# Optimization experiments

Measured on AMD Instinct MI355X. Metric: run time of the kernel, lower is better.

The kernel has to match this reference:

```python
import jax, jax.numpy as jnp
import numpy as np

K = 7
G = 16
PAD = K // 2
EPS = 1e-5


def setup_inputs() -> dict:
    key = jax.random.key(0)
    ks = jax.random.split(key, 8)
    C = 256
    Cr = C // 4  # ratio=4 bottleneck
    inputs = jax.random.normal(ks[0], (4, C, 56, 56), dtype=jnp.float32)
    W1 = jax.random.normal(ks[1], (Cr, C), dtype=jnp.float32) * 0.05
    b1 = jax.random.normal(ks[2], (Cr,), dtype=jnp.float32) * 0.05
    gamma = jax.random.normal(ks[3], (Cr,), dtype=jnp.float32) * 0.1 + 1.0
    beta = jax.random.normal(ks[4], (Cr,), dtype=jnp.float32) * 0.1
    mean = jax.random.normal(ks[5], (Cr,), dtype=jnp.float32) * 0.1
    var = jax.random.uniform(ks[6], (Cr,), dtype=jnp.float32) * 0.5 + 0.5
    W2 = jax.random.normal(ks[7], (G * K * K, Cr), dtype=jnp.float32) * 0.05
    b2 = jnp.zeros((G * K * K,), dtype=jnp.float32)
    return {"inputs": inputs, "W1": W1, "b1": b1, "gamma": gamma,
            "beta": beta, "mean": mean, "var": var, "W2": W2, "b2": b2}


def reference(inputs, W1, b1, gamma, beta, mean, var, W2, b2):
    B, C, H, W = inputs.shape
    Cg = C // G
    # kernel-generation branch: 1x1 conv -> BN (eval stats) -> relu -> 1x1 conv
    t = jnp.einsum('bchw,oc->bohw', inputs, W1) + b1[None, :, None, None]
    scale = gamma / jnp.sqrt(var + EPS)
    t = t * scale[None, :, None, None] + (beta - mean * scale)[None, :, None, None]
    t = jax.nn.relu(t)
    w = jnp.einsum('bchw,oc->bohw', t, W2) + b2[None, :, None, None]
    w = w.reshape(B, G, K * K, H, W)  # per-pixel kernel
    # involution: accumulate shifted slices instead of materializing unfold
    xp = jnp.pad(inputs, ((0, 0), (0, 0), (PAD, PAD), (PAD, PAD)))
    xg = xp.reshape(B, G, Cg, H + 2 * PAD, W + 2 * PAD)
    out = jnp.zeros((B, G, Cg, H, W), dtype=inputs.dtype)
    k = 0
    for i in range(K):
        for j in range(K):
            out = out + xg[:, :, :, i:i + H, j:j + W] * w[:, :, k][:, :, None, :, :]
            k += 1
    return out.reshape(B, C, H, W)
```

## Files before the change

kernel.cpp:

```cpp
#include <hip/hip_runtime.h>

#define HW    3136
#define HDIM  56
#define CIN   256
#define CR    64
#define NG    16
#define KK    49
#define BEPS  1e-5f

#define RB     2
#define NBAND  28
#define CHALF  28
#define WSTR   60
#define XR     8
#define XC     36
#define XCG    16
#define XTOT   (XR * XCG * XC)

typedef __attribute__((ext_vector_type(8))) short short8;
typedef __attribute__((ext_vector_type(4))) float f32x4;

__device__ __forceinline__ unsigned short f2bf(float f) {
    union { float f; unsigned u; } v; v.f = f;
    unsigned r = (v.u + 0x7FFFu + ((v.u >> 16) & 1u)) >> 16;
    return (unsigned short)r;
}

__global__ __launch_bounds__(256) void k0_prep(
    const float* __restrict__ W1, const float* __restrict__ b1,
    const float* __restrict__ gamma, const float* __restrict__ beta,
    const float* __restrict__ mean, const float* __restrict__ var,
    const float* __restrict__ W2,
    unsigned short* __restrict__ W1b, unsigned short* __restrict__ W2bT,
    float* __restrict__ b1f)
{
    int idx = blockIdx.x * 256 + threadIdx.x;
    if (idx < CR * CIN) {
        int o = idx >> 8;
        float s = gamma[o] * rsqrtf(var[o] + BEPS);
        W1b[idx] = f2bf(W1[idx] * s);
    } else if (idx < CR * CIN + NG * 64 * 64) {
        int j = idx - CR * CIN;
        int c = j & 63, tap = (j >> 6) & 63, g = j >> 12;
        float v = (tap < KK) ? W2[(g * KK + tap) * CR + c] : 0.f;
        W2bT[j] = f2bf(v);
    } else if (idx < CR * CIN + NG * 64 * 64 + CR) {
        int o = idx - CR * CIN - NG * 64 * 64;
        float s = gamma[o] * rsqrtf(var[o] + BEPS);
        b1f[o] = b1[o] * s + beta[o] - mean[o] * s;
    }
}

__global__ __launch_bounds__(128) void k1_gemm(
    const float* __restrict__ x, const unsigned short* __restrict__ W1b,
    const float* __restrict__ b1f, unsigned short* __restrict__ t_bf)
{
    __shared__ float red[64 * 17];

    const int tid = threadIdx.x;
    const int b = blockIdx.y;
    const int lane = tid & 63, l15 = lane & 15, q = lane >> 4;
    const int wid = tid >> 6;
    const int pxb = blockIdx.x * 16;
    const int kb = wid * 128;

    const float* xp = x + (size_t)b * CIN * HW + pxb + l15;

    f32x4 acc[4];
#pragma unroll
    for (int nt = 0; nt < 4; nt++) acc[nt] = (f32x4){0.f, 0.f, 0.f, 0.f};

#pragma unroll
    for (int kc = 0; kc < 4; kc++) {
        short8 af;
#pragma unroll
        for (int j = 0; j < 8; j++) {
            float xv = xp[(size_t)(kb + kc * 32 + q * 8 + j) * HW];
            af[j] = (short)f2bf(xv);
        }
#pragma unroll
        for (int nt = 0; nt < 4; nt++) {
            short8 bf = *(const short8*)&W1b[(size_t)(16 * nt + l15) * CIN + kb + kc * 32 + q * 8];
            acc[nt] = __builtin_amdgcn_mfma_f32_16x16x32_bf16(af, bf, acc[nt], 0, 0, 0);
        }
    }

    if (wid == 1) {
#pragma unroll
        for (int nt = 0; nt < 4; nt++)
#pragma unroll
            for (int r = 0; r < 4; r++)
                red[lane * 17 + nt * 4 + r] = acc[nt][r];
    }
    __syncthreads();
    if (wid == 0) {
#pragma unroll
        for (int nt = 0; nt < 4; nt++) {
            float bias = b1f[16 * nt + l15];
#pragma unroll
            for (int r = 0; r < 4; r++) {
                int px = pxb + 4 * q + r;
                float v = acc[nt][r] + red[lane * 17 + nt * 4 + r] + bias;
                t_bf[((size_t)b * HW + px) * CR + 16 * nt + l15] = f2bf(fmaxf(v, 0.f));
            }
        }
    }
}

__global__ __launch_bounds__(256, 5) void k2_fused(
    const float* __restrict__ x, const unsigned short* __restrict__ t_bf,
    const unsigned short* __restrict__ W2bT, const float* __restrict__ b2,
    float* __restrict__ out)
{
    __shared__ float w_lds[KK * WSTR];
    __shared__ float x_lds[XTOT];

    const int tid = threadIdx.x;
    const int band = blockIdx.x >> 1, chalf = blockIdx.x & 1;
    const int g = blockIdx.y, b = blockIdx.z;
    const int h0 = band * RB, c0 = chalf * CHALF;
    const int lane = tid & 63, l15 = lane & 15, q = lane >> 4;
    const int wid = tid >> 6;

#pragma unroll
    for (int it = 0; it < 18; it++) {
        int i = it * 256 + tid;
        int col = i % XC; int t2 = i / XC; int cg = t2 & 15; int rowx = t2 >> 4;
        int hy = h0 - 3 + rowx, xc = c0 + col - 4;
        float v = 0.f;
        if (hy >= 0 && hy < HDIM && xc >= 0 && xc < HDIM)
            v = x[((size_t)b * CIN + g * 16 + cg) * HW + hy * HDIM + xc];
        x_lds[i] = v;
    }

    {
        short8 bfr[4][2];
#pragma unroll
        for (int nt = 0; nt < 4; nt++)
#pragma unroll
            for (int ks = 0; ks < 2; ks++)
                bfr[nt][ks] = *(const short8*)&W2bT[((size_t)g * 64 + 16 * nt + l15) * 64 + ks * 32 + q * 8];
        float b2v[4];
#pragma unroll
        for (int nt = 0; nt < 4; nt++) {
            int tap = 16 * nt + l15;
            b2v[nt] = (tap < KK) ? b2[g * KK + tap] : 0.f;
        }
        const int row = wid >> 1, seg = wid & 1;
        int px = (h0 + row) * HDIM + c0 + seg * 16 + l15;
        if (px > HW - 1) px = HW - 1;
        const unsigned short* tp = &t_bf[((size_t)b * HW + px) * CR];
        short8 a0 = *(const short8*)&tp[q * 8];
        short8 a1 = *(const short8*)&tp[32 + q * 8];
        const int cl = seg * 16 + 4 * q;
#pragma unroll
        for (int nt = 0; nt < 4; nt++) {
            f32x4 acc = (f32x4){0.f, 0.f, 0.f, 0.f};
            acc = __builtin_amdgcn_mfma_f32_16x16x32_bf16(a0, bfr[nt][0], acc, 0, 0, 0);
            acc = __builtin_amdgcn_mfma_f32_16x16x32_bf16(a1, bfr[nt][1], acc, 0, 0, 0);
            int tap = 16 * nt + l15;
            if (tap < KK && cl < CHALF) {
                *(float4*)&w_lds[tap * WSTR + row * CHALF + cl] =
                    make_float4(acc[0] + b2v[nt], acc[1] + b2v[nt],
                                acc[2] + b2v[nt], acc[3] + b2v[nt]);
            }
        }
    }
    __syncthreads();

    if (tid < 224) {
        const int cg   = tid & 15;
        const int rq   = tid >> 4;
        const int row  = rq & 1;
        const int quad = rq >> 1;
        const int colb = quad * 4, h = h0 + row;

        float acc[4] = {0.f, 0.f, 0.f, 0.f};

#pragma unroll
        for (int di = 0; di < 7; di++) {
            float wv[7][4];
#pragma unroll
            for (int dj = 0; dj < 7; dj++) {
                float4 wq = *(const float4*)&w_lds[(di * 7 + dj) * WSTR + row * CHALF + colb];
                wv[dj][0] = wq.x; wv[dj][1] = wq.y; wv[dj][2] = wq.z; wv[dj][3] = wq.w;
            }
            const float* xr = &x_lds[((row + di) * 16 + cg) * XC + colb];
            float4 A  = *(const float4*)&xr[0];
            float4 Bv = *(const float4*)&xr[4];
            float4 Cv = *(const float4*)&xr[8];
            float win[12] = {A.x, A.y, A.z, A.w, Bv.x, Bv.y, Bv.z, Bv.w,
                             Cv.x, Cv.y, Cv.z, Cv.w};
#pragma unroll
            for (int dj = 0; dj < 7; dj++)
#pragma unroll
                for (int kk = 0; kk < 4; kk++)
                    acc[kk] += win[kk + dj + 1] * wv[dj][kk];
        }
        float* op = &out[((size_t)b * CIN + g * 16 + cg) * HW + h * HDIM + c0 + colb];
        *(float4*)op = make_float4(acc[0], acc[1], acc[2], acc[3]);
    }
}

extern "C" void kernel_launch(void* const* d_in, const int* in_sizes, int n_in,
                              void* d_out, int out_size, void* d_ws, size_t ws_size,
                              hipStream_t stream) {
    const float* x     = (const float*)d_in[0];
    const float* W1    = (const float*)d_in[1];
    const float* b1    = (const float*)d_in[2];
    const float* gamma = (const float*)d_in[3];
    const float* beta  = (const float*)d_in[4];
    const float* mean  = (const float*)d_in[5];
    const float* var   = (const float*)d_in[6];
    const float* W2    = (const float*)d_in[7];
    const float* b2    = (const float*)d_in[8];
    float* out = (float*)d_out;

    unsigned short* t_bf = (unsigned short*)d_ws;
    unsigned short* W1b  = t_bf + (size_t)4 * HW * CR;
    unsigned short* W2bT = W1b + CR * CIN;
    float* b1f           = (float*)(W2bT + NG * 64 * 64);

    int n_k0 = CR * CIN + NG * 64 * 64 + CR;
    k0_prep<<<(n_k0 + 255) / 256, 256, 0, stream>>>(
        W1, b1, gamma, beta, mean, var, W2, W1b, W2bT, b1f);

    dim3 g1(HW / 16, 4);
    k1_gemm<<<g1, 128, 0, stream>>>(x, W1b, b1f, t_bf);

    dim3 g2(NBAND * 2, NG, 4);
    k2_fused<<<g2, 256, 0, stream>>>(x, t_bf, W2bT, b2, out);
}
```

Baseline: 127.9 us.

## Fold weight prep into GEMM kernel and vectorize involution halo loads

After: 111.6 us (median of 2 runs). -12.7%, faster.

```diff
diff --git a/kernel.cpp b/kernel.cpp
--- a/kernel.cpp
+++ b/kernel.cpp
@@ -16,6 +16,9 @@
 #define XC     36
 #define XCG    16
 #define XTOT   (XR * XCG * XC)
+#define NSLOT  1152
+#define K1X    (HW / 16)
+#define K1PREP 32
 
 typedef __attribute__((ext_vector_type(8))) short short8;
 typedef __attribute__((ext_vector_type(4))) float f32x4;
@@ -26,39 +29,31 @@
     return (unsigned short)r;
 }
 
-__global__ __launch_bounds__(256) void k0_prep(
-    const float* __restrict__ W1, const float* __restrict__ b1,
-    const float* __restrict__ gamma, const float* __restrict__ beta,
-    const float* __restrict__ mean, const float* __restrict__ var,
-    const float* __restrict__ W2,
-    unsigned short* __restrict__ W1b, unsigned short* __restrict__ W2bT,
-    float* __restrict__ b1f)
+__global__ __launch_bounds__(128) void k1_gemm(
+    const float* __restrict__ x, const float* __restrict__ W1,
+    const float* __restrict__ b1, const float* __restrict__ gamma,
+    const float* __restrict__ beta, const float* __restrict__ mean,
+    const float* __restrict__ var, const float* __restrict__ W2,
+    unsigned short* __restrict__ t_bf, unsigned short* __restrict__ W2bT)
 {
-    int idx = blockIdx.x * 256 + threadIdx.x;
-    if (idx < CR * CIN) {
-        int o = idx >> 8;
-        float s = gamma[o] * rsqrtf(var[o] + BEPS);
-        W1b[idx] = f2bf(W1[idx] * s);
-    } else if (idx < CR * CIN + NG * 64 * 64) {
-        int j = idx - CR * CIN;
-        int c = j & 63, tap = (j >> 6) & 63, g = j >> 12;
-        float v = (tap < KK) ? W2[(g * KK + tap) * CR + c] : 0.f;
-        W2bT[j] = f2bf(v);
-    } else if (idx < CR * CIN + NG * 64 * 64 + CR) {
-        int o = idx - CR * CIN - NG * 64 * 64;
-        float s = gamma[o] * rsqrtf(var[o] + BEPS);
-        b1f[o] = b1[o] * s + beta[o] - mean[o] * s;
-    }
-}
-
-__global__ __launch_bounds__(128) void k1_gemm(
-    const float* __restrict__ x, const unsigned short* __restrict__ W1b,
-    const float* __restrict__ b1f, unsigned short* __restrict__ t_bf)
-{
-    __shared__ float red[64 * 17];
-
     const int tid = threadIdx.x;
     const int b = blockIdx.y;
+
+    if (blockIdx.x >= K1X) {
+        if (b) return;
+        int i = (blockIdx.x - K1X) * 128 + tid;
+#pragma unroll
+        for (int r = 0; r < 16; r++) {
+            int j = r * 4096 + i;
+            int c = j & 63, tap = (j >> 6) & 63, g = j >> 12;
+            float v = (tap < KK) ? W2[((size_t)g * KK + tap) * CR + c] : 0.f;
+            W2bT[j] = f2bf(v);
+        }
+        return;
+    }
+
+    __shared__ float red[64 * 17];
+
     const int lane = tid & 63, l15 = lane & 15, q = lane >> 4;
     const int wid = tid >> 6;
     const int pxb = blockIdx.x * 16;
@@ -66,6 +61,15 @@
 
     const float* xp = x + (size_t)b * CIN * HW + pxb + l15;
 
+    float sc[4], bias[4];
+#pragma unroll
+    for (int nt = 0; nt < 4; nt++) {
+        int o = 16 * nt + l15;
+        float s = gamma[o] * rsqrtf(var[o] + BEPS);
+        sc[nt] = s;
+        bias[nt] = b1[o] * s + beta[o] - mean[o] * s;
+    }
+
     f32x4 acc[4];
 #pragma unroll
     for (int nt = 0; nt < 4; nt++) acc[nt] = (f32x4){0.f, 0.f, 0.f, 0.f};
@@ -74,13 +78,18 @@
     for (int kc = 0; kc < 4; kc++) {
         short8 af;
 #pragma unroll
-        for (int j = 0; j < 8; j++) {
-            float xv = xp[(size_t)(kb + kc * 32 + q * 8 + j) * HW];
-            af[j] = (short)f2bf(xv);
-        }
+        for (int j = 0; j < 8; j++)
+            af[j] = (short)f2bf(xp[(size_t)(kb + kc * 32 + q * 8 + j) * HW]);
 #pragma unroll
         for (int nt = 0; nt < 4; nt++) {
-            short8 bf = *(const short8*)&W1b[(size_t)(16 * nt + l15) * CIN + kb + kc * 32 + q * 8];
+            const float* wp = &W1[(size_t)(16 * nt + l15) * CIN + kb + kc * 32 + q * 8];
+            float4 wa = *(const float4*)wp;
+            float4 wb = *(const float4*)(wp + 4);
+            short8 bf;
+            bf[0] = (short)f2bf(wa.x * sc[nt]); bf[1] = (short)f2bf(wa.y * sc[nt]);
+            bf[2] = (short)f2bf(wa.z * sc[nt]); bf[3] = (short)f2bf(wa.w * sc[nt]);
+            bf[4] = (short)f2bf(wb.x * sc[nt]); bf[5] = (short)f2bf(wb.y * sc[nt]);
+            bf[6] = (short)f2bf(wb.z * sc[nt]); bf[7] = (short)f2bf(wb.w * sc[nt]);
             acc[nt] = __builtin_amdgcn_mfma_f32_16x16x32_bf16(af, bf, acc[nt], 0, 0, 0);
         }
     }
@@ -96,11 +105,10 @@
     if (wid == 0) {
 #pragma unroll
         for (int nt = 0; nt < 4; nt++) {
-            float bias = b1f[16 * nt + l15];
 #pragma unroll
             for (int r = 0; r < 4; r++) {
                 int px = pxb + 4 * q + r;
-                float v = acc[nt][r] + red[lane * 17 + nt * 4 + r] + bias;
+                float v = acc[nt][r] + red[lane * 17 + nt * 4 + r] + bias[nt];
                 t_bf[((size_t)b * HW + px) * CR + 16 * nt + l15] = f2bf(fmaxf(v, 0.f));
             }
         }
@@ -122,37 +130,43 @@
     const int lane = tid & 63, l15 = lane & 15, q = lane >> 4;
     const int wid = tid >> 6;
 
-#pragma unroll
-    for (int it = 0; it < 18; it++) {
-        int i = it * 256 + tid;
-        int col = i % XC; int t2 = i / XC; int cg = t2 & 15; int rowx = t2 >> 4;
-        int hy = h0 - 3 + rowx, xc = c0 + col - 4;
-        float v = 0.f;
-        if (hy >= 0 && hy < HDIM && xc >= 0 && xc < HDIM)
-            v = x[((size_t)b * CIN + g * 16 + cg) * HW + hy * HDIM + xc];
-        x_lds[i] = v;
+    short8 bfr[4][2];
+#pragma unroll
+    for (int nt = 0; nt < 4; nt++)
+#pragma unroll
+        for (int ks = 0; ks < 2; ks++)
+            bfr[nt][ks] = *(const short8*)&W2bT[((size_t)g * 64 + 16 * nt + l15) * 64 + ks * 32 + q * 8];
+
+    const int arow = wid >> 1, aseg = wid & 1;
+    int apx = (h0 + arow) * HDIM + c0 + aseg * 16 + l15;
+    if (apx > HW - 1) apx = HW - 1;
+    const unsigned short* tp = &t_bf[((size_t)b * HW + apx) * CR];
+    short8 a0 = *(const short8*)&tp[q * 8];
+    short8 a1 = *(const short8*)&tp[32 + q * 8];
+
+    float b2v[4];
+#pragma unroll
+    for (int nt = 0; nt < 4; nt++) {
+        int tap = 16 * nt + l15;
+        b2v[nt] = (tap < KK) ? b2[g * KK + tap] : 0.f;
+    }
+
+    float4 xv[5];
+#pragma unroll
+    for (int it = 0; it < 5; it++) {
+        xv[it] = make_float4(0.f, 0.f, 0.f, 0.f);
+        if (it < 4 || tid < 128) {
+            int idx = it * 256 + tid;
+            int s = idx % 9, rc = idx / 9;
+            int cg = rc & 15, rowx = rc >> 4;
+            int hy = h0 - 3 + rowx, gx = c0 + 4 * s - 4;
+            if (hy >= 0 && hy < HDIM && gx >= 0 && gx <= HDIM - 4)
+                xv[it] = *(const float4*)&x[((size_t)b * CIN + g * 16 + cg) * HW + hy * HDIM + gx];
+        }
     }
 
     {
-        short8 bfr[4][2];
-#pragma unroll
-        for (int nt = 0; nt < 4; nt++)
-#pragma unroll
-            for (int ks = 0; ks < 2; ks++)
-                bfr[nt][ks] = *(const short8*)&W2bT[((size_t)g * 64 + 16 * nt + l15) * 64 + ks * 32 + q * 8];
-        float b2v[4];
-#pragma unroll
-        for (int nt = 0; nt < 4; nt++) {
-            int tap = 16 * nt + l15;
-            b2v[nt] = (tap < KK) ? b2[g * KK + tap] : 0.f;
-        }
-        const int row = wid >> 1, seg = wid & 1;
-        int px = (h0 + row) * HDIM + c0 + seg * 16 + l15;
-        if (px > HW - 1) px = HW - 1;
-        const unsigned short* tp = &t_bf[((size_t)b * HW + px) * CR];
-        short8 a0 = *(const short8*)&tp[q * 8];
-        short8 a1 = *(const short8*)&tp[32 + q * 8];
-        const int cl = seg * 16 + 4 * q;
+        const int cl = aseg * 16 + 4 * q;
 #pragma unroll
         for (int nt = 0; nt < 4; nt++) {
             f32x4 acc = (f32x4){0.f, 0.f, 0.f, 0.f};
@@ -160,10 +174,18 @@
             acc = __builtin_amdgcn_mfma_f32_16x16x32_bf16(a1, bfr[nt][1], acc, 0, 0, 0);
             int tap = 16 * nt + l15;
             if (tap < KK && cl < CHALF) {
-                *(float4*)&w_lds[tap * WSTR + row * CHALF + cl] =
+                *(float4*)&w_lds[tap * WSTR + arow * CHALF + cl] =
                     make_float4(acc[0] + b2v[nt], acc[1] + b2v[nt],
                                 acc[2] + b2v[nt], acc[3] + b2v[nt]);
             }
+        }
+    }
+
+#pragma unroll
+    for (int it = 0; it < 5; it++) {
+        if (it < 4 || tid < 128) {
+            int idx = it * 256 + tid;
+            *(float4*)&x_lds[idx * 4] = xv[it];
         }
     }
     __syncthreads();
@@ -217,16 +239,11 @@
     float* out = (float*)d_out;
 
     unsigned short* t_bf = (unsigned short*)d_ws;
-    unsigned short* W1b  = t_bf + (size_t)4 * HW * CR;
-    unsigned short* W2bT = W1b + CR * CIN;
-    float* b1f           = (float*)(W2bT + NG * 64 * 64);
-
-    int n_k0 = CR * CIN + NG * 64 * 64 + CR;
-    k0_prep<<<(n_k0 + 255) / 256, 256, 0, stream>>>(
-        W1, b1, gamma, beta, mean, var, W2, W1b, W2bT, b1f);
-
-    dim3 g1(HW / 16, 4);
-    k1_gemm<<<g1, 128, 0, stream>>>(x, W1b, b1f, t_bf);
+    unsigned short* W2bT = t_bf + (size_t)4 * HW * CR;
+
+    dim3 g1(K1X + K1PREP, 4);
+    k1_gemm<<<g1, 128, 0, stream>>>(x, W1, b1, gamma, beta, mean, var, W2,
+                                    t_bf, W2bT);
 
     dim3 g2(NBAND * 2, NG, 4);
     k2_fused<<<g2, 256, 0, stream>>>(x, t_bf, W2bT, b2, out);
```
